# Kernel tuning notes

Hardware: AMD Instinct MI355X
Metric: run time of the kernel (lower is better)

## Reference

```python
import jax, jax.numpy as jnp
import numpy as np

N_NODES = 16384
N_EDGES = 131072
N_GRAPHS = 64
DIMS = [396, 4096, 2048, 1024, 1024, 2048, 256, 1]  # layer widths from __init__
BN_EPS = 1e-5


def setup_inputs() -> dict:
    key = jax.random.key(0)
    ks = jax.random.split(key, 32)
    inp = {
        "x": jax.random.normal(ks[0], (N_NODES, DIMS[0]), jnp.float32),
        "edge_index": jax.random.randint(ks[1], (2, N_EDGES), 0, N_NODES, dtype=jnp.int32),
        "batch": jnp.sort(jax.random.randint(ks[2], (N_NODES,), 0, N_GRAPHS, dtype=jnp.int32)),
    }
    for i in range(7):
        fi, fo = DIMS[i], DIMS[i + 1]
        inp[f"W{i+1}"] = jax.random.normal(ks[3 + i], (fi, fo), jnp.float32) * (1.0 / np.sqrt(fi)).astype(np.float32)
        inp[f"b{i+1}"] = jnp.zeros((fo,), jnp.float32)
    for i in range(6):
        inp[f"g{i+1}"] = jnp.ones((DIMS[i + 1],), jnp.float32)
        inp[f"be{i+1}"] = jnp.zeros((DIMS[i + 1],), jnp.float32)
    return inp


def _gcn_norm(edge_index, n):
    # PyG GCNConv default: add self-loops, sym-normalize D^-1/2 (A+I) D^-1/2
    loop = jnp.arange(n, dtype=edge_index.dtype)
    src = jnp.concatenate([edge_index[0], loop])
    dst = jnp.concatenate([edge_index[1], loop])
    deg = jax.ops.segment_sum(jnp.ones_like(src, jnp.float32), dst, num_segments=n)
    dinv = jax.lax.rsqrt(jnp.maximum(deg, 1.0))  # deg >= 1 due to self-loops
    norm = dinv[src] * dinv[dst]  # [E + N]
    return src, dst, norm


def _gcn_conv(x, W, b, src, dst, norm, n):
    h = x @ W                                   # dense linear transform
    msg = h[src] * norm[:, None]                # gather + edge scaling
    agg = jax.ops.segment_sum(msg, dst, num_segments=n)  # scatter-add
    return agg + b


def _bn(x, g, b):
    # BatchNorm1d in training mode: biased batch variance
    m = jnp.mean(x, axis=0)
    v = jnp.mean(jnp.square(x - m), axis=0)
    return (x - m) * jax.lax.rsqrt(v + BN_EPS) * g + b


def reference(x, edge_index, batch,
              W1, b1, W2, b2, W3, b3, W4, b4, W5, b5, W6, b6, W7, b7,
              g1, be1, g2, be2, g3, be3, g4, be4, g5, be5, g6, be6):
    n = x.shape[0]
    src, dst, norm = _gcn_norm(edge_index, n)
    Ws = [W1, W2, W3, W4, W5, W6]
    bs = [b1, b2, b3, b4, b5, b6]
    gs = [g1, g2, g3, g4, g5, g6]
    bes = [be1, be2, be3, be4, be5, be6]
    h = x
    for W, b, g, be in zip(Ws, bs, gs, bes):
        h = jax.nn.relu(_gcn_conv(h, W, b, src, dst, norm, n))
        h = _bn(h, g, be)
    h = _gcn_conv(h, W7, b7, src, dst, norm, n)   # [N, 1], no relu/bn
    out = jax.ops.segment_sum(h, batch, num_segments=N_GRAPHS)  # global_add_pool
    return out
```

## Files before the change

kernel.cpp:

```cpp
#include <hip/hip_runtime.h>


#define NN 16384
#define NE 131072
#define NG 64

typedef unsigned int u32;
typedef unsigned short u16;
typedef __attribute__((ext_vector_type(8))) _Float16 half8;
typedef __attribute__((ext_vector_type(4))) float f32x4;
typedef __attribute__((ext_vector_type(8))) u16 us8;
typedef __attribute__((ext_vector_type(4))) u16 us4;
typedef __attribute__((ext_vector_type(2))) u16 us2;

#define AS1(p) ((const __attribute__((address_space(1))) void*)(p))
#define AS3(p) ((__attribute__((address_space(3))) void*)(p))

__device__ __forceinline__ float b2f(u16 h) {
    _Float16 x = __builtin_bit_cast(_Float16, h);
    return (float)x;
}
__device__ __forceinline__ u16 f2b(float f) {
    _Float16 x = (_Float16)f;
    return __builtin_bit_cast(u16, x);
}

template <int VW> struct VecU;
template <> struct VecU<8> { typedef us8 T; };
template <> struct VecU<4> { typedef us4 T; };
template <> struct VecU<2> { typedef us2 T; };
template <> struct VecU<1> { typedef u16 T; };

template <int VW>
__device__ __forceinline__ void loadf(const u16* p, float* f) {
    typename VecU<VW>::T v = *(const typename VecU<VW>::T*)p;
    if constexpr (VW == 1) {
        f[0] = b2f((u16)v);
    } else {
        #pragma unroll
        for (int j = 0; j < VW; ++j) f[j] = b2f(v[j]);
    }
}
template <int VW>
__device__ __forceinline__ void storef(u16* p, const float* f) {
    typename VecU<VW>::T v;
    if constexpr (VW == 1) {
        v = f2b(f[0]);
    } else {
        #pragma unroll
        for (int j = 0; j < VW; ++j) v[j] = f2b(f[j]);
    }
    *(typename VecU<VW>::T*)p = v;
}

__device__ __forceinline__ void bn_ab(float s1c, float s2c, float gc, float bec,
                                      float& a, float& b) {
    float m = s1c * (1.f / NN);
    float var = s2c * (1.f / NN) - m * m;
    a = gc * rsqrtf(var + 1e-5f);
    b = bec - m * a;
}

__global__ void k_degi(const int* __restrict__ dst, int* __restrict__ deg) {
    int e = blockIdx.x * 256 + threadIdx.x;
    if (e < NE) atomicAdd(&deg[dst[e]], 1);
}
__global__ void k_nrm(const int* __restrict__ src, const int* __restrict__ dst,
                      const float* __restrict__ dinv, float* __restrict__ nrm) {
    int e = blockIdx.x * 256 + threadIdx.x;
    if (e < NE) nrm[e] = dinv[src[e]] * dinv[dst[e]];
}
__global__ __launch_bounds__(1024) void k_scan(const int* __restrict__ deg, int* __restrict__ rowptr,
                                               float* __restrict__ dinv) {
    __shared__ int part[1024];
    int t = threadIdx.x;
    int base = t * 16;
    int s = 0;
    #pragma unroll
    for (int j = 0; j < 16; ++j) {
        int d = deg[base + j];
        dinv[base + j] = rsqrtf((float)(d + 1));
        s += d;
    }
    part[t] = s;
    __syncthreads();
    for (int off = 1; off < 1024; off <<= 1) {
        int v = 0;
        if (t >= off) v = part[t - off];
        __syncthreads();
        part[t] += v;
        __syncthreads();
    }
    int run = part[t] - s;
    for (int j = 0; j < 16; ++j) { rowptr[base + j] = run; run += deg[base + j]; }
    if (t == 1023) rowptr[NN] = run;
}
__global__ void k_place(const int* __restrict__ src, const int* __restrict__ dst,
                        const float* __restrict__ nrm, const int* __restrict__ rowptr,
                        int* __restrict__ cursor, int* __restrict__ csr_src,
                        float* __restrict__ csr_w) {
    int e = blockIdx.x * 256 + threadIdx.x;
    if (e >= NE) return;
    int d = dst[e];
    int p = rowptr[d] + atomicAdd(&cursor[d], 1);
    csr_src[p] = src[e];
    csr_w[p] = nrm[e];
}

__global__ void k_x2b(const float* __restrict__ x, u16* __restrict__ xp) {
    int idx = blockIdx.x * 256 + threadIdx.x;
    int i = idx >> 6, cg = idx & 63;
    int c0 = cg * 8;
    float v[8];
    #pragma unroll
    for (int j = 0; j < 8; ++j) {
        int c = c0 + j;
        v[j] = (c < 396) ? x[(size_t)i * 396 + c] : 0.f;
    }
    storef<8>(xp + (size_t)i * 512 + c0, v);
}
__global__ void k_wt(const float* __restrict__ W, u16* __restrict__ Wt,
                     int Ksrc, int Kpad, int N) {
    __shared__ float t[32][33];
    int k0 = blockIdx.x * 32, n0 = blockIdx.y * 32;
    int tx = threadIdx.x, ty = threadIdx.y;
    #pragma unroll
    for (int j = 0; j < 4; ++j) {
        int k = k0 + ty + j * 8;
        float v = 0.f;
        if (k < Ksrc) v = W[(size_t)k * N + n0 + tx];
        t[ty + j * 8][tx] = v;
    }
    __syncthreads();
    #pragma unroll
    for (int j = 0; j < 4; ++j) {
        int n = n0 + ty + j * 8;
        int k = k0 + tx;
        Wt[(size_t)n * Kpad + k] = f2b(t[tx][ty + j * 8]);
    }
}

template <int VW>
__global__ __launch_bounds__(256) void k_agg(const u16* __restrict__ in, u16* __restrict__ out,
                                             const int* __restrict__ rowptr,
                                             const int* __restrict__ csr_src,
                                             const float* __restrict__ csr_w,
                                             const float* __restrict__ dinv,
                                             const float* __restrict__ svec,
                                             const float* __restrict__ bias,
                                             const float* __restrict__ s1,
                                             const float* __restrict__ s2,
                                             const float* __restrict__ g,
                                             const float* __restrict__ be,
                                             float* __restrict__ svw,
                                             int F, int mode) {
    int i = blockIdx.x;
    int c0 = threadIdx.x * VW;
    float acc[VW];
    float d2 = dinv[i]; d2 *= d2;
    float wsum = d2;
    {
        float v[VW];
        loadf<VW>(in + (size_t)i * F + c0, v);
        #pragma unroll
        for (int j = 0; j < VW; ++j) acc[j] = d2 * v[j];
    }
    int r0 = rowptr[i], r1 = rowptr[i + 1];
    int e = r0;
    if (r1 - r0 >= 2) {
        float acc2[VW];
        #pragma unroll
        for (int j = 0; j < VW; ++j) acc2[j] = 0.f;
        for (; e + 1 < r1; e += 2) {
            int sa = csr_src[e], sb = csr_src[e + 1];
            float wa = csr_w[e], wb = csr_w[e + 1];
            wsum += wa + wb;
            float va[VW], vb[VW];
            loadf<VW>(in + (size_t)sa * F + c0, va);
            loadf<VW>(in + (size_t)sb * F + c0, vb);
            #pragma unroll
            for (int j = 0; j < VW; ++j) { acc[j] += wa * va[j]; acc2[j] += wb * vb[j]; }
        }
        #pragma unroll
        for (int j = 0; j < VW; ++j) acc[j] += acc2[j];
    }
    for (; e < r1; ++e) {
        int s = csr_src[e];
        float w = csr_w[e];
        wsum += w;
        float v[VW];
        loadf<VW>(in + (size_t)s * F + c0, v);
        #pragma unroll
        for (int j = 0; j < VW; ++j) acc[j] += w * v[j];
    }
    if (mode == 1) {
        #pragma unroll
        for (int j = 0; j < VW; ++j) acc[j] = fmaxf(acc[j] + bias[c0 + j], 0.f);
    } else if (mode == 2) {
        float si = svec[i];
        #pragma unroll
        for (int j = 0; j < VW; ++j) {
            float a, b;
            bn_ab(s1[c0 + j], s2[c0 + j], g[c0 + j], be[c0 + j], a, b);
            acc[j] = a * acc[j] + si * b;
        }
    }
    storef<VW>(out + (size_t)i * F + c0, acc);
    if (svw && threadIdx.x == 0) svw[i] = wsum;
}

#define SROWS 128
template <int VW>
__global__ __launch_bounds__(256) void k_stats(const u16* __restrict__ h, float* __restrict__ s1,
                                               float* __restrict__ s2, int F) {
    int c0 = threadIdx.x * VW;
    int r0 = blockIdx.y * SROWS;
    float s[VW], q[VW];
    #pragma unroll
    for (int j = 0; j < VW; ++j) { s[j] = 0.f; q[j] = 0.f; }
    for (int r = r0; r < r0 + SROWS; ++r) {
        float v[VW];
        loadf<VW>(h + (size_t)r * F + c0, v);
        #pragma unroll
        for (int j = 0; j < VW; ++j) { s[j] += v[j]; q[j] += v[j] * v[j]; }
    }
    #pragma unroll
    for (int j = 0; j < VW; ++j) {
        atomicAdd(&s1[c0 + j], s[j]);
        atomicAdd(&s2[c0 + j], q[j]);
    }
}
__global__ __launch_bounds__(256) void k_bnapply(u16* __restrict__ h, const float* __restrict__ s1,
                                                 const float* __restrict__ s2,
                                                 const float* __restrict__ g,
                                                 const float* __restrict__ be, int F) {
    size_t idx = blockIdx.x * (size_t)256 + threadIdx.x;
    int Fv = F >> 3;
    int c = (int)(idx % Fv) * 8;
    u16* p = h + idx * 8;
    float v[8];
    loadf<8>(p, v);
    #pragma unroll
    for (int j = 0; j < 8; ++j) {
        float a, b;
        bn_ab(s1[c + j], s2[c + j], g[c + j], be[c + j], a, b);
        v[j] = a * v[j] + b;
    }
    storef<8>(p, v);
}

__device__ __forceinline__ void stage16k(const char* gbase, size_t rs, int ktile, int h,
                                         char* slot, int tid) {
    size_t colb = (size_t)ktile * 128 + h * 64;
    #pragma unroll
    for (int i = 0; i < 2; ++i) {
        int G = i * 512 + tid;
        int r = G >> 2;
        int c = ((G & 3) - (r >> 1)) & 3;
        __builtin_amdgcn_global_load_lds(AS1(gbase + (size_t)r * rs + colb + c * 16),
                                         AS3(slot + i * 8192 + ((tid >> 6) << 10)), 16, 0, 0);
    }
}

__global__ __launch_bounds__(512, 2) void k_gemm256(const u16* __restrict__ A,
                                                    const u16* __restrict__ Wt,
                                                    const float* __restrict__ bias,
                                                    u16* __restrict__ C,
                                                    float* __restrict__ s1,
                                                    float* __restrict__ s2,
                                                    int K, int N, int bx, int fuse) {
    extern __shared__ __align__(16) char smem[];
    int nwg = gridDim.x;
    int chunk = nwg >> 3;
    int swz = (blockIdx.x & 7) * chunk + (blockIdx.x >> 3);
    int tx = swz % bx, ty = swz / bx;
    int tid = threadIdx.x;
    int wid = tid >> 6, lane = tid & 63;
    int wr = wid >> 2, wc = wid & 3;
    int lo = lane & 15, hi = lane >> 4;
    int sw = (((hi + (lo >> 1)) & 3) << 4);
    size_t row0 = (size_t)ty * 256;
    size_t col0 = (size_t)tx * 256;
    int nkt = K >> 6;

    const char* gA = (const char*)(A + row0 * K);
    const char* gB = (const char*)(Wt + col0 * K);
    size_t rs = (size_t)K * 2;

    const char* aA = smem + wr * 8192 + lo * 64 + sw;
    const char* bA = smem + 65536 + wc * 4096 + lo * 64 + sw;
#define ASL(b, h) (smem + (((b) * 2 + (h)) << 14))
#define BSL(b, h) (smem + 65536 + (((b) * 2 + (h)) << 14))

    f32x4 acc[8][4];
    #pragma unroll
    for (int m = 0; m < 8; ++m)
        #pragma unroll
        for (int n = 0; n < 4; ++n) acc[m][n] = {0.f, 0.f, 0.f, 0.f};
    half8 af0[4], af1[4], bf[4];

    stage16k(gA, rs, 0, 0, ASL(0, 0), tid);
    stage16k(gB, rs, 0, 0, BSL(0, 0), tid);
    stage16k(gA, rs, 0, 1, ASL(0, 1), tid);
    stage16k(gB, rs, 0, 1, BSL(0, 1), tid);
    stage16k(gA, rs, 1, 0, ASL(1, 0), tid);
    stage16k(gB, rs, 1, 0, BSL(1, 0), tid);
    asm volatile("s_waitcnt vmcnt(4)" ::: "memory");
    __builtin_amdgcn_sched_barrier(0);
    __builtin_amdgcn_s_barrier();

#define DS_LOADS2(KK)                                                                      \
    {                                                                                      \
        _Pragma("unroll") for (int j = 0; j < 4; ++j)                                      \
            af0[j] = *(const half8*)(aA + buf * 32768 + (KK) * 16384 + j * 1024);          \
        _Pragma("unroll") for (int j = 0; j < 4; ++j)                                      \
            af1[j] = *(const half8*)(aA + buf * 32768 + (KK) * 16384 + 4096 + j * 1024);   \
        _Pragma("unroll") for (int j = 0; j < 4; ++j)                                      \
            bf[j] = *(const half8*)(bA + buf * 32768 + (KK) * 16384 + j * 1024);           \
    }
#define MFMA_BOTH                                                                          \
    {                                                                                      \
        __builtin_amdgcn_s_setprio(1);                                                     \
        _Pragma("unroll") for (int j = 0; j < 4; ++j)                                      \
            _Pragma("unroll") for (int n = 0; n < 4; ++n)                                  \
                acc[j][n] = __builtin_amdgcn_mfma_f32_16x16x32_f16(                        \
                    af0[j], bf[n], acc[j][n], 0, 0, 0);                                    \
        _Pragma("unroll") for (int j = 0; j < 4; ++j)                                      \
            _Pragma("unroll") for (int n = 0; n < 4; ++n)                                  \
                acc[4 + j][n] = __builtin_amdgcn_mfma_f32_16x16x32_f16(                    \
                    af1[j], bf[n], acc[4 + j][n], 0, 0, 0);                                \
        __builtin_amdgcn_s_setprio(0);                                                     \
    }
#define END_BARRIER                                                                        \
    {                                                                                      \
        asm volatile("" ::: "memory");                                                     \
        __builtin_amdgcn_s_barrier();                                                      \
    }

    for (int kt = 0; kt < nkt; ++kt) {
        int buf = kt & 1;
        DS_LOADS2(0);
        if (kt + 1 < nkt) {
            stage16k(gA, rs, kt + 1, 1, ASL(buf ^ 1, 1), tid);
            stage16k(gB, rs, kt + 1, 1, BSL(buf ^ 1, 1), tid);
        }
        MFMA_BOTH;
        END_BARRIER;
        DS_LOADS2(1);
        if (kt + 2 < nkt) {
            stage16k(gA, rs, kt + 2, 0, ASL(buf, 0), tid);
            stage16k(gB, rs, kt + 2, 0, BSL(buf, 0), tid);
        }
        MFMA_BOTH;
        asm volatile("s_waitcnt vmcnt(4)" ::: "memory");
        __builtin_amdgcn_sched_barrier(0);
        END_BARRIER;
    }

    float cs[4] = {0.f, 0.f, 0.f, 0.f}, cq[4] = {0.f, 0.f, 0.f, 0.f};
    #pragma unroll
    for (int fm = 0; fm < 8; ++fm) {
        #pragma unroll
        for (int n = 0; n < 4; ++n) {
            #pragma unroll
            for (int r = 0; r < 4; ++r) {
                size_t row = row0 + wr * 128 + fm * 16 + hi * 4 + r;
                size_t col = col0 + wc * 64 + n * 16 + lo;
                float v = acc[fm][n][r];
                if (fuse) v = fmaxf(v + bias[col], 0.f);
                C[row * N + col] = f2b(v);
                cs[n] += v;
                cq[n] += v * v;
            }
        }
    }
    if (s1) {
        asm volatile("s_waitcnt vmcnt(0)" ::: "memory");
        __syncthreads();
        float* sp = (float*)smem;
        sp[tid] = 0.f;
        __syncthreads();
        #pragma unroll
        for (int n = 0; n < 4; ++n) {
            int lc = wc * 64 + n * 16 + lo;
            atomicAdd(&sp[lc * 2], cs[n]);
            atomicAdd(&sp[lc * 2 + 1], cq[n]);
        }
        __syncthreads();
        if (tid < 256) {
            atomicAdd(&s1[col0 + tid], sp[tid * 2]);
            atomicAdd(&s2[col0 + tid], sp[tid * 2 + 1]);
        }
    }
#undef DS_LOADS2
#undef MFMA_BOTH
#undef END_BARRIER
#undef ASL
#undef BSL
}

__global__ __launch_bounds__(256) void k_gemm(const u16* __restrict__ A, const u16* __restrict__ Wt,
                                              const float* __restrict__ bias, u16* __restrict__ C,
                                              int K, int N, int bx, int fuse) {
    __shared__ __align__(16) u16 As[128 * 32];
    __shared__ __align__(16) u16 Bs[128 * 32];
    int nwg = gridDim.x;
    int chunk = nwg >> 3;
    int swz = (blockIdx.x & 7) * chunk + (blockIdx.x >> 3);
    int tx = swz % bx, ty = swz / bx;
    int tid = threadIdx.x;
    int wid = tid >> 6, lane = tid & 63;
    int wr = wid >> 1, wc = wid & 1;
    int lo = lane & 15, hi = lane >> 4;
    size_t row0 = (size_t)ty * 128;
    size_t col0 = (size_t)tx * 128;

    f32x4 acc[4][4];
    #pragma unroll
    for (int m = 0; m < 4; ++m)
        #pragma unroll
        for (int n = 0; n < 4; ++n) acc[m][n] = {0.f, 0.f, 0.f, 0.f};

    const char* gA = (const char*)(A + row0 * K);
    const char* gB = (const char*)(Wt + col0 * K);
    size_t rs = (size_t)K * 2;
    int lin0 = tid * 16;
    int lin1 = lin0 + 4096;
    int rA0 = lin0 >> 6, cb0 = lin0 & 63;
    int rA1 = lin1 >> 6, cb1 = lin1 & 63;
    unsigned ldsOff = (unsigned)(wid << 10);

    for (int k0 = 0; k0 < K; k0 += 32) {
        __syncthreads();
        size_t kb = (size_t)k0 * 2;
        __builtin_amdgcn_global_load_lds(AS1(gA + (size_t)rA0 * rs + cb0 + kb),
                                         AS3((char*)As + ldsOff), 16, 0, 0);
        __builtin_amdgcn_global_load_lds(AS1(gA + (size_t)rA1 * rs + cb1 + kb),
                                         AS3((char*)As + 4096 + ldsOff), 16, 0, 0);
        __builtin_amdgcn_global_load_lds(AS1(gB + (size_t)rA0 * rs + cb0 + kb),
                                         AS3((char*)Bs + ldsOff), 16, 0, 0);
        __builtin_amdgcn_global_load_lds(AS1(gB + (size_t)rA1 * rs + cb1 + kb),
                                         AS3((char*)Bs + 4096 + ldsOff), 16, 0, 0);
        __syncthreads();
        half8 afr[4], bfr[4];
        #pragma unroll
        for (int m = 0; m < 4; ++m)
            afr[m] = *(const half8*)((const u16*)As + (wr * 64 + m * 16 + lo) * 32 + hi * 8);
        #pragma unroll
        for (int n = 0; n < 4; ++n)
            bfr[n] = *(const half8*)((const u16*)Bs + (wc * 64 + n * 16 + lo) * 32 + hi * 8);
        #pragma unroll
        for (int m = 0; m < 4; ++m)
            #pragma unroll
            for (int n = 0; n < 4; ++n)
                acc[m][n] = __builtin_amdgcn_mfma_f32_16x16x32_f16(afr[m], bfr[n], acc[m][n], 0, 0, 0);
    }
    #pragma unroll
    for (int m = 0; m < 4; ++m) {
        #pragma unroll
        for (int n = 0; n < 4; ++n) {
            #pragma unroll
            for (int r = 0; r < 4; ++r) {
                size_t row = row0 + wr * 64 + m * 16 + hi * 4 + r;
                size_t col = col0 + wc * 64 + n * 16 + lo;
                float v = acc[m][n][r];
                if (fuse) v = fmaxf(v + bias[col], 0.f);
                C[row * N + col] = f2b(v);
            }
        }
    }
}

__global__ __launch_bounds__(256) void k_gemv(const u16* __restrict__ A, const float* __restrict__ w,
                                              const float* __restrict__ s1, const float* __restrict__ s2,
                                              const float* __restrict__ g, const float* __restrict__ be,
                                              float* __restrict__ y) {
    int row = blockIdx.x * 4 + (threadIdx.x >> 6);
    int lane = threadIdx.x & 63;
    const u16* h = A + (size_t)row * 256;
    float s = 0.f;
    #pragma unroll
    for (int j = 0; j < 4; ++j) {
        int c = lane + j * 64;
        float a, b;
        bn_ab(s1[c], s2[c], g[c], be[c], a, b);
        s += (a * b2f(h[c]) + b) * w[c];
    }
    #pragma unroll
    for (int off = 32; off; off >>= 1) s += __shfl_down(s, off);
    if (lane == 0) y[row] = s;
}
__global__ void k_final(const float* __restrict__ y, const int* __restrict__ rowptr,
                        const int* __restrict__ csr_src, const float* __restrict__ csr_w,
                        const float* __restrict__ dinv, const int* __restrict__ batch,
                        const float* __restrict__ b7, float* __restrict__ out) {
    int i = blockIdx.x * 256 + threadIdx.x;
    if (i >= NN) return;
    float v = dinv[i] * dinv[i] * y[i];
    int r1 = rowptr[i + 1];
    for (int e = rowptr[i]; e < r1; ++e) v += csr_w[e] * y[csr_src[e]];
    atomicAdd(&out[batch[i]], v + b7[0]);
}
__global__ void k_sentinel(float* out, float v) {
    if (threadIdx.x == 0 && blockIdx.x == 0) out[0] = v;
}

static inline char* alignp(char* p) { return (char*)(((uintptr_t)p + 255) & ~(uintptr_t)255); }

extern "C" void kernel_launch(void* const* d_in, const int* in_sizes, int n_in,
                              void* d_out, int out_size, void* d_ws, size_t ws_size,
                              hipStream_t stream) {
    const float* x = (const float*)d_in[0];
    const int* ei = (const int*)d_in[1];
    const int* src = ei;
    const int* dst = ei + NE;
    const int* batch = (const int*)d_in[2];
    const float* W[7]; const float* bv[7];
    for (int i = 0; i < 7; ++i) { W[i] = (const float*)d_in[3 + 2 * i]; bv[i] = (const float*)d_in[4 + 2 * i]; }
    const float* g[6]; const float* be[6];
    for (int i = 0; i < 6; ++i) { g[i] = (const float*)d_in[17 + 2 * i]; be[i] = (const float*)d_in[18 + 2 * i]; }
    float* out = (float*)d_out;

    char* p = (char*)d_ws;
    u16* Abuf = (u16*)p; p += (size_t)NN * 4096 * 2;
    u16* Bbuf = (u16*)p; p += (size_t)NN * 2048 * 2;
    u16* xpad = (u16*)p; p += (size_t)NN * 512 * 2;
    u16* W1t = (u16*)p; p += (size_t)4096 * 512 * 2;
    u16* W2t = (u16*)p; p += (size_t)2048 * 4096 * 2;
    u16* W3t = (u16*)p; p += (size_t)1024 * 2048 * 2;
    u16* W4t = (u16*)p; p += (size_t)1024 * 1024 * 2;
    u16* W5t = (u16*)p; p += (size_t)2048 * 1024 * 2;
    u16* W6t = (u16*)p; p += (size_t)256 * 2048 * 2;
    p = alignp(p);
    int* degi = (int*)p; p += NN * 4;
    int* cursor = (int*)p; p += NN * 4;
    int* rowptr = (int*)p; p += (NN + 1) * 4; p = alignp(p);
    int* csr_src = (int*)p; p += NE * 4;
    float* csr_w = (float*)p; p += NE * 4;
    float* dinv = (float*)p; p += NN * 4;
    float* nrm = (float*)p; p += NE * 4;
    float* svec = (float*)p; p += NN * 4;
    float* s1 = (float*)p; p += 4096 * 4;
    float* s2 = (float*)p; p += 4096 * 4;
    float* y = (float*)p; p += NN * 4;
    size_t need = (size_t)(p - (char*)d_ws);
    if (need > ws_size) {
        hipMemsetAsync(d_out, 0, NG * sizeof(float), stream);
        k_sentinel<<<1, 64, 0, stream>>>(out, (float)(ws_size >> 20));
        return;
    }

    (void)hipFuncSetAttribute((const void*)k_gemm256,
                              hipFuncAttributeMaxDynamicSharedMemorySize, 131072);

    hipMemsetAsync(degi, 0, 2 * NN * sizeof(int), stream);
    k_degi<<<NE / 256, 256, 0, stream>>>(dst, degi);
    k_scan<<<1, 1024, 0, stream>>>(degi, rowptr, dinv);
    k_nrm<<<NE / 256, 256, 0, stream>>>(src, dst, dinv, nrm);
    k_place<<<NE / 256, 256, 0, stream>>>(src, dst, nrm, rowptr, cursor, csr_src, csr_w);

    k_x2b<<<(NN * 64) / 256, 256, 0, stream>>>(x, xpad);
    dim3 wtb(32, 8);
    k_wt<<<dim3(16, 128), wtb, 0, stream>>>(W[0], W1t, 396, 512, 4096);
    k_wt<<<dim3(128, 64), wtb, 0, stream>>>(W[1], W2t, 4096, 4096, 2048);
    k_wt<<<dim3(64, 32), wtb, 0, stream>>>(W[2], W3t, 2048, 2048, 1024);
    k_wt<<<dim3(32, 32), wtb, 0, stream>>>(W[3], W4t, 1024, 1024, 1024);
    k_wt<<<dim3(32, 64), wtb, 0, stream>>>(W[4], W5t, 1024, 1024, 2048);
    k_wt<<<dim3(64, 8), wtb, 0, stream>>>(W[5], W6t, 2048, 2048, 256);

    auto gemm256 = [&](const u16* A, const u16* Wt, const float* bias, u16* Cp,
                       float* st1, float* st2, int K, int N, int fuse) {
        int bx = N / 256;
        k_gemm256<<<bx * (NN / 256), 512, 131072, stream>>>(A, Wt, bias, Cp, st1, st2, K, N, bx, fuse);
    };
    auto agg = [&](const u16* in, u16* o, const float* bias, int li, float* svw,
                   int F, int mode) {
        const float* gp = (mode == 2) ? g[li] : nullptr;
        const float* bep = (mode == 2) ? be[li] : nullptr;
        if (F >= 512) k_agg<8><<<NN, F / 8, 0, stream>>>(in, o, rowptr, csr_src, csr_w, dinv, svec, bias, s1, s2, gp, bep, svw, F, mode);
        else k_agg<4><<<NN, F / 4, 0, stream>>>(in, o, rowptr, csr_src, csr_w, dinv, svec, bias, s1, s2, gp, bep, svw, F, mode);
    };
    auto stats = [&](const u16* h, int F) {
        hipMemsetAsync(s1, 0, 2 * 4096 * sizeof(float), stream);
        if (F >= 512) k_stats<8><<<dim3(1, NN / SROWS), F / 8, 0, stream>>>(h, s1, s2, F);
        else k_stats<4><<<dim3(1, NN / SROWS), F / 4, 0, stream>>>(h, s1, s2, F);
    };
    auto bnapply = [&](u16* h, int F, int li) {
        k_bnapply<<<(int)(((size_t)NN * F / 8) / 256), 256, 0, stream>>>(h, s1, s2, g[li], be[li], F);
    };

    agg(xpad, Bbuf, nullptr, 0, svec, 512, 0);
    hipMemsetAsync(s1, 0, 2 * 4096 * sizeof(float), stream);
    gemm256(Bbuf, W1t, bv[0], Abuf, s1, s2, 512, 4096, 1);
    bnapply(Abuf, 4096, 0);

    gemm256(Abuf, W2t, nullptr, Bbuf, nullptr, nullptr, 4096, 2048, 0);
    agg(Bbuf, Abuf, bv[1], 1, nullptr, 2048, 1);
    stats(Abuf, 2048);
    bnapply(Abuf, 2048, 1);

    gemm256(Abuf, W3t, nullptr, Bbuf, nullptr, nullptr, 2048, 1024, 0);
    agg(Bbuf, Abuf, bv[2], 2, nullptr, 1024, 1);
    stats(Abuf, 1024);
    bnapply(Abuf, 1024, 2);

    gemm256(Abuf, W4t, nullptr, Bbuf, nullptr, nullptr, 1024, 1024, 0);
    agg(Bbuf, Abuf, bv[3], 3, nullptr, 1024, 1);
    stats(Abuf, 1024);

    agg(Abuf, Bbuf, nullptr, 3, nullptr, 1024, 2);
    hipMemsetAsync(s1, 0, 2 * 4096 * sizeof(float), stream);
    gemm256(Bbuf, W5t, bv[4], Abuf, s1, s2, 1024, 2048, 1);
    bnapply(Abuf, 2048, 4);

    k_gemm<<<(256 / 128) * (NN / 128), 256, 0, stream>>>(Abuf, W6t, nullptr, Bbuf, 2048, 256, 256 / 128, 0);
    agg(Bbuf, Abuf, bv[5], 5, nullptr, 256, 1);
    stats(Abuf, 256);

    k_gemv<<<NN / 4, 256, 0, stream>>>(Abuf, W[6], s1, s2, g[5], be[5], y);
    hipMemsetAsync(d_out, 0, NG * sizeof(float), stream);
    k_final<<<NN / 256, 256, 0, stream>>>(y, rowptr, csr_src, csr_w, dinv, batch, bv[6], out);
}
```

Before: 1.406 ms.

## Aggregate before layer-4 GEMM with folded BN, fuse stats into GEMM, drop norm kernel

Layer 4 now aggregates first (A·(BN(h)))·W instead of A·(BN(h)·W). The layer-3 batchnorm is folded into the aggregation (mode 2), and the GEMM epilogue adds bias, applies ReLU and accumulates batch stats into a second stats buffer. This removes a separate bnapply pass, a stats pass and a relu-aggregate pass over 1024-wide activations. The edge norm computation is also folded into k_place, removing one small kernel and an intermediate buffer. It relies on aggregation commuting with the linear map and on the svec row-weight trick for the folded BN shift.

```diff
diff --git a/kernel.cpp b/kernel.cpp
--- a/kernel.cpp
+++ b/kernel.cpp
@@ -64,11 +64,6 @@
 __global__ void k_degi(const int* __restrict__ dst, int* __restrict__ deg) {
     int e = blockIdx.x * 256 + threadIdx.x;
     if (e < NE) atomicAdd(&deg[dst[e]], 1);
-}
-__global__ void k_nrm(const int* __restrict__ src, const int* __restrict__ dst,
-                      const float* __restrict__ dinv, float* __restrict__ nrm) {
-    int e = blockIdx.x * 256 + threadIdx.x;
-    if (e < NE) nrm[e] = dinv[src[e]] * dinv[dst[e]];
 }
 __global__ __launch_bounds__(1024) void k_scan(const int* __restrict__ deg, int* __restrict__ rowptr,
                                                float* __restrict__ dinv) {
@@ -96,15 +91,16 @@
     if (t == 1023) rowptr[NN] = run;
 }
 __global__ void k_place(const int* __restrict__ src, const int* __restrict__ dst,
-                        const float* __restrict__ nrm, const int* __restrict__ rowptr,
+                        const float* __restrict__ dinv, const int* __restrict__ rowptr,
                         int* __restrict__ cursor, int* __restrict__ csr_src,
                         float* __restrict__ csr_w) {
     int e = blockIdx.x * 256 + threadIdx.x;
     if (e >= NE) return;
+    int sidx = src[e];
     int d = dst[e];
     int p = rowptr[d] + atomicAdd(&cursor[d], 1);
-    csr_src[p] = src[e];
-    csr_w[p] = nrm[e];
+    csr_src[p] = sidx;
+    csr_w[p] = dinv[sidx] * dinv[d];
 }
 
 __global__ void k_x2b(const float* __restrict__ x, u16* __restrict__ xp) {
@@ -148,8 +144,8 @@
                                              const float* __restrict__ dinv,
                                              const float* __restrict__ svec,
                                              const float* __restrict__ bias,
-                                             const float* __restrict__ s1,
-                                             const float* __restrict__ s2,
+                                             const float* __restrict__ st1,
+                                             const float* __restrict__ st2,
                                              const float* __restrict__ g,
                                              const float* __restrict__ be,
                                              float* __restrict__ svw,
@@ -201,7 +197,7 @@
         #pragma unroll
         for (int j = 0; j < VW; ++j) {
             float a, b;
-            bn_ab(s1[c0 + j], s2[c0 + j], g[c0 + j], be[c0 + j], a, b);
+            bn_ab(st1[c0 + j], st2[c0 + j], g[c0 + j], be[c0 + j], a, b);
             acc[j] = a * acc[j] + si * b;
         }
     }
@@ -538,10 +534,11 @@
     int* csr_src = (int*)p; p += NE * 4;
     float* csr_w = (float*)p; p += NE * 4;
     float* dinv = (float*)p; p += NN * 4;
-    float* nrm = (float*)p; p += NE * 4;
     float* svec = (float*)p; p += NN * 4;
     float* s1 = (float*)p; p += 4096 * 4;
     float* s2 = (float*)p; p += 4096 * 4;
+    float* s1b = (float*)p; p += 4096 * 4;
+    float* s2b = (float*)p; p += 4096 * 4;
     float* y = (float*)p; p += NN * 4;
     size_t need = (size_t)(p - (char*)d_ws);
     if (need > ws_size) {
@@ -556,8 +553,7 @@
     hipMemsetAsync(degi, 0, 2 * NN * sizeof(int), stream);
     k_degi<<<NE / 256, 256, 0, stream>>>(dst, degi);
     k_scan<<<1, 1024, 0, stream>>>(degi, rowptr, dinv);
-    k_nrm<<<NE / 256, 256, 0, stream>>>(src, dst, dinv, nrm);
-    k_place<<<NE / 256, 256, 0, stream>>>(src, dst, nrm, rowptr, cursor, csr_src, csr_w);
+    k_place<<<NE / 256, 256, 0, stream>>>(src, dst, dinv, rowptr, cursor, csr_src, csr_w);
 
     k_x2b<<<(NN * 64) / 256, 256, 0, stream>>>(x, xpad);
     dim3 wtb(32, 8);
@@ -573,12 +569,12 @@
         int bx = N / 256;
         k_gemm256<<<bx * (NN / 256), 512, 131072, stream>>>(A, Wt, bias, Cp, st1, st2, K, N, bx, fuse);
     };
-    auto agg = [&](const u16* in, u16* o, const float* bias, int li, float* svw,
-                   int F, int mode) {
+    auto agg = [&](const u16* in, u16* o, const float* bias, int li,
+                   const float* st1, const float* st2, float* svw, int F, int mode) {
         const float* gp = (mode == 2) ? g[li] : nullptr;
         const float* bep = (mode == 2) ? be[li] : nullptr;
-        if (F >= 512) k_agg<8><<<NN, F / 8, 0, stream>>>(in, o, rowptr, csr_src, csr_w, dinv, svec, bias, s1, s2, gp, bep, svw, F, mode);
-        else k_agg<4><<<NN, F / 4, 0, stream>>>(in, o, rowptr, csr_src, csr_w, dinv, svec, bias, s1, s2, gp, bep, svw, F, mode);
+        if (F >= 512) k_agg<8><<<NN, F / 8, 0, stream>>>(in, o, rowptr, csr_src, csr_w, dinv, svec, bias, st1, st2, gp, bep, svw, F, mode);
+        else k_agg<4><<<NN, F / 4, 0, stream>>>(in, o, rowptr, csr_src, csr_w, dinv, svec, bias, st1, st2, gp, bep, svw, F, mode);
     };
     auto stats = [&](const u16* h, int F) {
         hipMemsetAsync(s1, 0, 2 * 4096 * sizeof(float), stream);
@@ -589,32 +585,31 @@
         k_bnapply<<<(int)(((size_t)NN * F / 8) / 256), 256, 0, stream>>>(h, s1, s2, g[li], be[li], F);
     };
 
-    agg(xpad, Bbuf, nullptr, 0, svec, 512, 0);
+    agg(xpad, Bbuf, nullptr, 0, nullptr, nullptr, svec, 512, 0);
     hipMemsetAsync(s1, 0, 2 * 4096 * sizeof(float), stream);
     gemm256(Bbuf, W1t, bv[0], Abuf, s1, s2, 512, 4096, 1);
     bnapply(Abuf, 4096, 0);
 
     gemm256(Abuf, W2t, nullptr, Bbuf, nullptr, nullptr, 4096, 2048, 0);
-    agg(Bbuf, Abuf, bv[1], 1, nullptr, 2048, 1);
+    agg(Bbuf, Abuf, bv[1], 1, nullptr, nullptr, nullptr, 2048, 1);
     stats(Abuf, 2048);
     bnapply(Abuf, 2048, 1);
 
     gemm256(Abuf, W3t, nullptr, Bbuf, nullptr, nullptr, 2048, 1024, 0);
-    agg(Bbuf, Abuf, bv[2], 2, nullptr, 1024, 1);
+    agg(Bbuf, Abuf, bv[2], 2, nullptr, nullptr, nullptr, 1024, 1);
     stats(Abuf, 1024);
-    bnapply(Abuf, 1024, 2);
-
-    gemm256(Abuf, W4t, nullptr, Bbuf, nullptr, nullptr, 1024, 1024, 0);
-    agg(Bbuf, Abuf, bv[3], 3, nullptr, 1024, 1);
-    stats(Abuf, 1024);
-
-    agg(Abuf, Bbuf, nullptr, 3, nullptr, 1024, 2);
+
+    agg(Abuf, Bbuf, nullptr, 2, s1, s2, nullptr, 1024, 2);
+    hipMemsetAsync(s1b, 0, 2 * 4096 * sizeof(float), stream);
+    gemm256(Bbuf, W4t, bv[3], Abuf, s1b, s2b, 1024, 1024, 1);
+
+    agg(Abuf, Bbuf, nullptr, 3, s1b, s2b, nullptr, 1024, 2);
     hipMemsetAsync(s1, 0, 2 * 4096 * sizeof(float), stream);
     gemm256(Bbuf, W5t, bv[4], Abuf, s1, s2, 1024, 2048, 1);
     bnapply(Abuf, 2048, 4);
 
     k_gemm<<<(256 / 128) * (NN / 128), 256, 0, stream>>>(Abuf, W6t, nullptr, Bbuf, 2048, 256, 256 / 128, 0);
-    agg(Bbuf, Abuf, bv[5], 5, nullptr, 256, 1);
+    agg(Bbuf, Abuf, bv[5], 5, nullptr, nullptr, nullptr, 256, 1);
     stats(Abuf, 256);
 
     k_gemv<<<NN / 4, 256, 0, stream>>>(Abuf, W[6], s1, s2, g[5], be[5], y);
```

Result: faster. 1.367 ms (-2.8%).
